# Kernel optimization log

Measured on AMD Instinct MI355X. Metric: run time of the kernel, lower is better.

The kernel has to match this reference:

```python
import jax, jax.numpy as jnp
import numpy as np

N_NODES = 200_000
BATCH = 131_072
D = 128          # memory_dim
E = 64           # edge_feat_dim
T = 64           # time_dim
P = 5            # num_prototypes
LN_EPS = 1e-4


def _xavier(key, shape):
    fan_in, fan_out = shape[-1], shape[-2] if len(shape) > 1 else shape[-1]
    lim = float(np.sqrt(6.0 / (fan_in + fan_out)))
    return jax.random.uniform(key, shape, jnp.float32, -lim, lim)


def _ln(x, g, b):
    mu = x.mean(-1, keepdims=True)
    var = ((x - mu) ** 2).mean(-1, keepdims=True)
    return (x - mu) * jax.lax.rsqrt(var + LN_EPS) * g + b


def setup_inputs() -> dict:
    key = jax.random.key(0)
    ks = jax.random.split(key, 14)
    return {
        "node_ids": jax.random.randint(ks[0], (BATCH,), 0, N_NODES),
        "edge_features": jax.random.normal(ks[1], (BATCH, E), jnp.float32),
        "t": jax.random.uniform(ks[2], (BATCH,), jnp.float32),
        "raw_memory": jax.random.normal(ks[3], (N_NODES, D), jnp.float32) * 0.01,
        "all_prototypes": _xavier(ks[4], (N_NODES, P, D)),
        "proto_ln_g": jnp.ones((D,), jnp.float32),
        "proto_ln_b": jnp.zeros((D,), jnp.float32),
        "time_w": jax.random.normal(ks[5], (T,), jnp.float32),
        "time_b": jnp.zeros((T,), jnp.float32),
        "edge_w": _xavier(ks[6], (D, E)),
        "edge_b": jnp.zeros((D,), jnp.float32),
        "query_w": _xavier(ks[7], (D, D + D + T)),
        "query_b": jnp.zeros((D,), jnp.float32),
        "cell_ln_g": jnp.ones((D,), jnp.float32),
        "cell_ln_b": jnp.zeros((D,), jnp.float32),
        "gate_w": _xavier(ks[8], (1, 2 * D + T)),
        "gate_b": jnp.ones((1,), jnp.float32),
        "temperature": jnp.ones((1,), jnp.float32) * 0.1,
    }


def reference(node_ids, edge_features, t, raw_memory, all_prototypes,
              proto_ln_g, proto_ln_b, time_w, time_b, edge_w, edge_b,
              query_w, query_b, cell_ln_g, cell_ln_b, gate_w, gate_b,
              temperature):
    # gather per-interaction state
    raw = raw_memory[node_ids]                                   # [B, D]
    protos = _ln(all_prototypes[node_ids], proto_ln_g, proto_ln_b)  # [B, P, D]
    # projections / time encoding (TimeEncoder: cos(Linear(t)))
    edge = edge_features @ edge_w.T + edge_b                     # [B, D]
    te = jnp.cos(t[:, None] * time_w[None, :] + time_b)          # [B, T]
    # query
    qi = jnp.concatenate([raw, edge, te], axis=-1)               # [B, 2D+T]
    query = jnp.tanh(_ln(qi @ query_w.T + query_b, cell_ln_g, cell_ln_b))
    # cosine similarity over P prototypes
    qn = query / jnp.clip(jnp.linalg.norm(query, axis=-1, keepdims=True), 1e-6)
    pn = protos / jnp.clip(jnp.linalg.norm(protos, axis=-1, keepdims=True), 1e-6)
    sim = jnp.einsum('bd,bpd->bp', qn, pn)
    sim = jnp.clip(sim, -30.0, 30.0)
    temp = jnp.clip(temperature, 0.05, 2.0)
    sim = sim / (temp + 1e-4)
    attn = jnp.nan_to_num(jax.nn.softmax(sim, axis=-1), nan=0.0, posinf=0.0, neginf=0.0)
    # candidate memory + gate
    cand = jnp.clip(jnp.einsum('bp,bpd->bd', attn, protos), -5.0, 5.0)
    gi = jnp.clip(jnp.concatenate([raw, cand, te], axis=-1), -100.0, 100.0)
    gate = jax.nn.sigmoid(gi @ gate_w.T + gate_b)                # [B, 1]
    upd = (1.0 - gate) * raw + gate * cand
    upd = jnp.clip(_ln(upd, cell_ln_g, cell_ln_b), -10.0, 10.0)
    return upd
```

## Files before the change

kernel.cpp:

```cpp
#include <hip/hip_runtime.h>

#define D 128
#define EDIM 64
#define TDIM 64
#define KTOT 256
#define NP 5
#define LN_EPS 1e-4f
#define WSB_OFF 33024

typedef float v4f __attribute__((ext_vector_type(4)));
typedef float f32x4 __attribute__((ext_vector_type(4)));
typedef short bf16x8 __attribute__((ext_vector_type(8)));

__device__ __forceinline__ float clipf(float x, float lo, float hi) {
    return fminf(fmaxf(x, lo), hi);
}

__device__ __forceinline__ unsigned short bf16rne(float x) {
    unsigned int u = __float_as_uint(x);
    unsigned int r = (u + 0x7fffu + ((u >> 16) & 1u)) >> 16;
    return (unsigned short)r;
}
__device__ __forceinline__ float bf16tof(unsigned short h) {
    return __uint_as_float(((unsigned int)h) << 16);
}

template <int CTRL>
__device__ __forceinline__ float dpp_addstep(float v) {
    int o = __builtin_amdgcn_update_dpp(0, __float_as_int(v), CTRL, 0xF, 0xF, true);
    return v + __int_as_float(o);
}
__device__ __forceinline__ float qred16(float v) {
    v = dpp_addstep<0xB1>(v);
    v = dpp_addstep<0x4E>(v);
    v = dpp_addstep<0x124>(v);
    v = dpp_addstep<0x128>(v);
    return v;
}

__global__ void k0_fold(const float* __restrict__ qw, const float* __restrict__ qb,
                        const float* __restrict__ ew, const float* __restrict__ eb,
                        const float* __restrict__ pg, const float* __restrict__ pb,
                        float* __restrict__ ws) {
    const int d = threadIdx.x;
    const int bk = blockIdx.x;
    float* Wt = ws;
    float* c0 = ws + KTOT * D;
    float* cc = c0 + D;
    if (bk < 128) {
        Wt[bk * D + d] = qw[d * 320 + bk];
    } else if (bk < 192) {
        const int e = bk - 128;
        const float4* qrow = (const float4*)(qw + d * 320 + 128);
        float s = 0.f;
        #pragma unroll
        for (int g = 0; g < 32; ++g) {
            float4 q = qrow[g];
            s = fmaf(q.x, ew[(4 * g + 0) * EDIM + e], s);
            s = fmaf(q.y, ew[(4 * g + 1) * EDIM + e], s);
            s = fmaf(q.z, ew[(4 * g + 2) * EDIM + e], s);
            s = fmaf(q.w, ew[(4 * g + 3) * EDIM + e], s);
        }
        Wt[bk * D + d] = s;
    } else if (bk < 256) {
        Wt[bk * D + d] = qw[d * 320 + 256 + (bk - 192)];
    } else if (bk == 256) {
        const float4* qrow = (const float4*)(qw + d * 320 + 128);
        const float4* eb4 = (const float4*)eb;
        float s = qb[d];
        #pragma unroll
        for (int g = 0; g < 32; ++g) {
            float4 q = qrow[g], e4 = eb4[g];
            s = fmaf(q.x, e4.x, s); s = fmaf(q.y, e4.y, s);
            s = fmaf(q.z, e4.z, s); s = fmaf(q.w, e4.w, s);
        }
        c0[d] = s;
    } else {
        if (d == 0) { float s = 0.f; for (int i = 0; i < D; ++i) s = fmaf(pg[i], pg[i], s); cc[0] = s; }
        if (d == 1) { float s = 0.f; for (int i = 0; i < D; ++i) s = fmaf(pg[i], pb[i], s); cc[1] = s; }
        if (d == 2) { float s = 0.f; for (int i = 0; i < D; ++i) s = fmaf(pb[i], pb[i], s); cc[2] = s; }
    }
}

__global__ void k0b_pack(float* __restrict__ ws) {
    const int kb = blockIdx.x >> 3;
    const int nt = blockIdx.x & 7;
    const int l = threadIdx.x;
    const float* Wt = ws;
    const int col = nt * 16 + (l & 15);
    const int kbase = kb * 32 + (l >> 4) * 8;
    bf16x8 hi, lo;
    #pragma unroll
    for (int j = 0; j < 8; ++j) {
        float x = Wt[(kbase + j) * D + col];
        unsigned short h = bf16rne(x);
        hi[j] = (short)h;
        lo[j] = (short)bf16rne(x - bf16tof(h));
    }
    bf16x8* outp = (bf16x8*)(ws + WSB_OFF);
    outp[((kb * 8 + nt) * 2 + 0) * 64 + l] = hi;
    outp[((kb * 8 + nt) * 2 + 1) * 64 + l] = lo;
}

__global__ __launch_bounds__(256, 3)
void k_fused(const int* __restrict__ nids, const float* __restrict__ ef,
             const float* __restrict__ tarr, const float* __restrict__ raw_mem,
             const float* __restrict__ protos,
             const float* __restrict__ pg, const float* __restrict__ pb,
             const float* __restrict__ tw, const float* __restrict__ tb,
             const float* __restrict__ cg, const float* __restrict__ cb,
             const float* __restrict__ gw, const float* __restrict__ gb,
             const float* __restrict__ temp, const float* __restrict__ ws,
             float* __restrict__ out, int Btot) {
    __shared__ bf16x8 Bs[1024];
    __shared__ float cst[960];

    const int tid = threadIdx.x;
    const int lane = tid & 63;
    const int wave = tid >> 6;
    const int m0 = blockIdx.x * 64 + wave * 16;
    const int col = lane & 15;
    const int kg = lane >> 4;

    if (tid < 128) {
        cst[tid] = gw[tid];
        cst[128 + tid] = gw[128 + tid];
    } else {
        const int u = tid - 128;
        if (u < 64) { cst[256 + u] = tw[u]; cst[320 + u] = tb[u]; }
        else        { cst[384 + u - 64] = gw[256 + u - 64]; }
    }

    const int elemA = min(m0 + col, Btot - 1);
    const int nidA = nids[elemA];
    const float* rawpA = raw_mem + (size_t)nidA * D + kg * 8;
    const float* efpA = ef + (size_t)elemA * EDIM + kg * 8;
    const float tvalA = tarr[elemA];
    const bf16x8* wbg = (const bf16x8*)(ws + WSB_OFF);

    f32x4 acc[8];
    #pragma unroll
    for (int nt = 0; nt < 8; ++nt) acc[nt] = (f32x4){0.f, 0.f, 0.f, 0.f};

    bf16x8 s0 = wbg[tid], s1 = wbg[256 + tid], s2 = wbg[512 + tid], s3 = wbg[768 + tid];
    v4f xa0 = *(const v4f*)rawpA;
    v4f xa1 = *(const v4f*)(rawpA + 4);

    #pragma unroll 1
    for (int kb = 0; kb < 8; ++kb) {
        __syncthreads();
        Bs[tid] = s0; Bs[256 + tid] = s1; Bs[512 + tid] = s2; Bs[768 + tid] = s3;
        __syncthreads();
        v4f xn0 = xa0, xn1 = xa1;
        if (kb < 7) {
            const int kn = kb + 1;
            const bf16x8* wn = wbg + kn * 1024;
            s0 = wn[tid]; s1 = wn[256 + tid]; s2 = wn[512 + tid]; s3 = wn[768 + tid];
            if (kn < 4) {
                xn0 = *(const v4f*)(rawpA + kn * 32);
                xn1 = *(const v4f*)(rawpA + kn * 32 + 4);
            } else if (kn < 6) {
                xn0 = *(const v4f*)(efpA + (kn - 4) * 32);
                xn1 = *(const v4f*)(efpA + (kn - 4) * 32 + 4);
            } else {
                const int u0 = (kn - 6) * 32 + kg * 8;
                v4f wa = *(const v4f*)(tw + u0);
                v4f wb2 = *(const v4f*)(tw + u0 + 4);
                v4f ba = *(const v4f*)(tb + u0);
                v4f bb2 = *(const v4f*)(tb + u0 + 4);
                #pragma unroll
                for (int j = 0; j < 4; ++j) xn0[j] = __cosf(fmaf(tvalA, wa[j], ba[j]));
                #pragma unroll
                for (int j = 0; j < 4; ++j) xn1[j] = __cosf(fmaf(tvalA, wb2[j], bb2[j]));
            }
        }
        bf16x8 ahi, alo;
        #pragma unroll
        for (int j = 0; j < 4; ++j) {
            unsigned short h = bf16rne(xa0[j]);
            ahi[j] = (short)h;
            alo[j] = (short)bf16rne(xa0[j] - bf16tof(h));
        }
        #pragma unroll
        for (int j = 0; j < 4; ++j) {
            unsigned short h = bf16rne(xa1[j]);
            ahi[4 + j] = (short)h;
            alo[4 + j] = (short)bf16rne(xa1[j] - bf16tof(h));
        }
        #pragma unroll
        for (int nt = 0; nt < 8; ++nt) {
            bf16x8 bhi = Bs[(nt * 2 + 0) * 64 + lane];
            bf16x8 blo = Bs[(nt * 2 + 1) * 64 + lane];
            acc[nt] = __builtin_amdgcn_mfma_f32_16x16x32_bf16(ahi, bhi, acc[nt], 0, 0, 0);
            acc[nt] = __builtin_amdgcn_mfma_f32_16x16x32_bf16(ahi, blo, acc[nt], 0, 0, 0);
            acc[nt] = __builtin_amdgcn_mfma_f32_16x16x32_bf16(alo, bhi, acc[nt], 0, 0, 0);
        }
        xa0 = xn0; xa1 = xn1;
    }

    {
        const float* c0 = ws + KTOT * D;
        #pragma unroll
        for (int j = 0; j < 8; ++j) {
            const float cv = c0[j * 16 + col];
            acc[j][0] += cv; acc[j][1] += cv; acc[j][2] += cv; acc[j][3] += cv;
        }
    }
    const float sbb = (ws + KTOT * D + D)[2];
    const float tempc = fminf(fmaxf(temp[0], 0.05f), 2.0f) + 1e-4f;
    const float its = 1.0f / tempc;
    const float gbias = gb[0];

    float pg8[8], pb8[8], cg8[8], cb8[8];
    #pragma unroll
    for (int j = 0; j < 8; ++j) {
        const int dd = j * 16 + col;
        pg8[j] = pg[dd]; pb8[j] = pb[dd];
        cg8[j] = cg[dd]; cb8[j] = cb[dd];
    }

    #pragma unroll
    for (int r = 0; r < 4; ++r) {
        const int erow = m0 + kg * 4 + r;
        const bool act = (erow < Btot);
        const int ebb = act ? erow : Btot - 1;
        const int nid = nids[ebb];
        const float* rawrow = raw_mem + (size_t)nid * D;
        const float* prow = protos + (size_t)nid * (NP * D);
        const float tval = tarr[ebb];

        float qv[8], rawv[8];
        #pragma unroll
        for (int j = 0; j < 8; ++j) {
            qv[j] = acc[j][r];
            rawv[j] = rawrow[j * 16 + col];
        }
        float pxv[NP][8];
        #pragma unroll
        for (int p = 0; p < NP; ++p) {
            #pragma unroll
            for (int j = 0; j < 8; ++j) pxv[p][j] = prow[p * D + j * 16 + col];
        }

        float gsum = 0.f;
        #pragma unroll
        for (int j = 0; j < 8; ++j)
            gsum = fmaf(cst[j * 16 + col], clipf(rawv[j], -100.f, 100.f), gsum);
        #pragma unroll
        for (int j = 0; j < 4; ++j) {
            const int u = col * 4 + j;
            gsum = fmaf(cst[384 + u], __cosf(fmaf(tval, cst[256 + u], cst[320 + u])), gsum);
        }

        float sx = 0.f;
        #pragma unroll
        for (int j = 0; j < 8; ++j) sx += qv[j];
        sx = qred16(sx);
        const float mu = sx * (1.f / D);
        float sv = 0.f;
        #pragma unroll
        for (int j = 0; j < 8; ++j) { float a = qv[j] - mu; sv = fmaf(a, a, sv); }
        sv = qred16(sv);
        const float rsq = __builtin_amdgcn_rsqf(sv * (1.f / D) + LN_EPS);

        float ssq = 0.f;
        #pragma unroll
        for (int j = 0; j < 8; ++j) {
            float x = fmaf((qv[j] - mu) * rsq, cg8[j], cb8[j]);
            float e2x = __expf(2.f * x);
            float th = 1.f - 2.f * __builtin_amdgcn_rcpf(e2x + 1.f);
            qv[j] = th;
            ssq = fmaf(th, th, ssq);
        }
        ssq = qred16(ssq);
        const float invq = __builtin_amdgcn_rcpf(fmaxf(sqrtf(ssq), 1e-6f));

        float aqg = 0.f, aqb = 0.f;
        #pragma unroll
        for (int j = 0; j < 8; ++j) {
            float qn = qv[j] * invq;
            float qg = qn * pg8[j];
            aqg += qg;
            aqb = fmaf(qn, pb8[j], aqb);
            qv[j] = qg;
        }
        aqg = qred16(aqg);
        aqb = qred16(aqb);

        float mups[NP], rsps[NP], simv[NP];
        #pragma unroll
        for (int p = 0; p < NP; ++p) {
            float s_x = 0.f, sxx = 0.f, sqgx = 0.f;
            #pragma unroll
            for (int j = 0; j < 8; ++j) {
                float x = pxv[p][j];
                s_x += x;
                sxx = fmaf(x, x, sxx);
                sqgx = fmaf(qv[j], x, sqgx);
            }
            s_x = qred16(s_x); sxx = qred16(sxx); sqgx = qred16(sqgx);
            const float mup = s_x * (1.f / D);
            const float varp = sxx * (1.f / D) - mup * mup;
            const float rsp = __builtin_amdgcn_rsqf(varp + LN_EPS);
            float sz2 = 0.f, szb = 0.f;
            #pragma unroll
            for (int j = 0; j < 8; ++j) {
                float z = (pxv[p][j] - mup) * pg8[j];
                sz2 = fmaf(z, z, sz2);
                szb = fmaf(z, pb8[j], szb);
            }
            sz2 = qred16(sz2); szb = qred16(szb);
            const float dot = fmaf(rsp, sqgx - mup * aqg, aqb);
            float nrm2 = fmaf(rsp * rsp, sz2, fmaf(2.f * rsp, szb, sbb));
            nrm2 = fmaxf(nrm2, 0.f);
            const float inv = __builtin_amdgcn_rcpf(fmaxf(sqrtf(nrm2), 1e-6f));
            mups[p] = mup;
            rsps[p] = rsp;
            simv[p] = clipf(dot * inv, -30.f, 30.f) * its;
        }

        float mx = fmaxf(fmaxf(fmaxf(simv[0], simv[1]), fmaxf(simv[2], simv[3])), simv[4]);
        float wp[NP];
        float Z = 0.f;
        #pragma unroll
        for (int p = 0; p < NP; ++p) { float ev = __expf(simv[p] - mx); wp[p] = ev; Z += ev; }
        const float iZ = 1.f / Z;
        float a0 = 0.f, a1 = 0.f;
        #pragma unroll
        for (int p = 0; p < NP; ++p) {
            float at = wp[p] * iZ;
            a0 += at;
            float w = at * rsps[p];
            a1 = fmaf(w, mups[p], a1);
            wp[p] = w;
        }

        float S8[8];
        #pragma unroll
        for (int j = 0; j < 8; ++j) S8[j] = 0.f;
        #pragma unroll
        for (int p = 0; p < NP; ++p) {
            #pragma unroll
            for (int j = 0; j < 8; ++j) S8[j] = fmaf(wp[p], pxv[p][j], S8[j]);
        }
        float gc = gsum;
        #pragma unroll
        for (int j = 0; j < 8; ++j) {
            float cnd = clipf(fmaf(pg8[j], S8[j] - a1, pb8[j] * a0), -5.f, 5.f);
            gc = fmaf(cst[128 + j * 16 + col], cnd, gc);
            S8[j] = cnd;
        }
        gc = qred16(gc);
        const float gpre = gc + gbias;
        const float gate = __builtin_amdgcn_rcpf(1.f + __expf(-gpre));

        float su = 0.f, ssu = 0.f;
        #pragma unroll
        for (int j = 0; j < 8; ++j) {
            float u = fmaf(gate, S8[j] - rawv[j], rawv[j]);
            S8[j] = u;
            su += u;
            ssu = fmaf(u, u, ssu);
        }
        su = qred16(su);
        ssu = qred16(ssu);
        const float muu = su * (1.f / D);
        const float varu = ssu * (1.f / D) - muu * muu;
        const float rsu = __builtin_amdgcn_rsqf(varu + LN_EPS);

        if (act) {
            float* orow = out + (size_t)erow * D;
            #pragma unroll
            for (int j = 0; j < 8; ++j) {
                orow[j * 16 + col] = clipf(fmaf((S8[j] - muu) * rsu, cg8[j], cb8[j]), -10.f, 10.f);
            }
        }
    }
}

extern "C" void kernel_launch(void* const* d_in, const int* in_sizes, int n_in,
                              void* d_out, int out_size, void* d_ws, size_t ws_size,
                              hipStream_t stream) {
    const int*   nids = (const int*)d_in[0];
    const float* ef   = (const float*)d_in[1];
    const float* t    = (const float*)d_in[2];
    const float* raw  = (const float*)d_in[3];
    const float* prot = (const float*)d_in[4];
    const float* pg   = (const float*)d_in[5];
    const float* pb   = (const float*)d_in[6];
    const float* tw   = (const float*)d_in[7];
    const float* tb   = (const float*)d_in[8];
    const float* ew   = (const float*)d_in[9];
    const float* eb   = (const float*)d_in[10];
    const float* qw   = (const float*)d_in[11];
    const float* qb   = (const float*)d_in[12];
    const float* cg   = (const float*)d_in[13];
    const float* cb   = (const float*)d_in[14];
    const float* gw   = (const float*)d_in[15];
    const float* gb   = (const float*)d_in[16];
    const float* temp = (const float*)d_in[17];
    float* ws  = (float*)d_ws;
    float* out = (float*)d_out;
    const int Btot = in_sizes[0];

    hipLaunchKernelGGL(k0_fold, dim3(258), dim3(128), 0, stream,
                       qw, qb, ew, eb, pg, pb, ws);
    hipLaunchKernelGGL(k0b_pack, dim3(64), dim3(64), 0, stream, ws);
    hipLaunchKernelGGL(k_fused, dim3((Btot + 63) / 64), dim3(256), 0, stream,
                       nids, ef, t, raw, prot, pg, pb, tw, tb, cg, cb, gw, gb, temp, ws, out, Btot);
}
```

Before: 120.5 us.

## Permute weight columns so each lane owns 8 contiguous features; vectorize epilogue loads

```diff
diff --git a/kernel.cpp b/kernel.cpp
--- a/kernel.cpp
+++ b/kernel.cpp
@@ -87,12 +87,12 @@
     const int nt = blockIdx.x & 7;
     const int l = threadIdx.x;
     const float* Wt = ws;
-    const int col = nt * 16 + (l & 15);
+    const int dlog = (l & 15) * 8 + nt;
     const int kbase = kb * 32 + (l >> 4) * 8;
     bf16x8 hi, lo;
     #pragma unroll
     for (int j = 0; j < 8; ++j) {
-        float x = Wt[(kbase + j) * D + col];
+        float x = Wt[(kbase + j) * D + dlog];
         unsigned short h = bf16rne(x);
         hi[j] = (short)h;
         lo[j] = (short)bf16rne(x - bf16tof(h));
@@ -113,7 +113,6 @@
              const float* __restrict__ temp, const float* __restrict__ ws,
              float* __restrict__ out, int Btot) {
     __shared__ bf16x8 Bs[1024];
-    __shared__ float cst[960];
 
     const int tid = threadIdx.x;
     const int lane = tid & 63;
@@ -121,15 +120,6 @@
     const int m0 = blockIdx.x * 64 + wave * 16;
     const int col = lane & 15;
     const int kg = lane >> 4;
-
-    if (tid < 128) {
-        cst[tid] = gw[tid];
-        cst[128 + tid] = gw[128 + tid];
-    } else {
-        const int u = tid - 128;
-        if (u < 64) { cst[256 + u] = tw[u]; cst[320 + u] = tb[u]; }
-        else        { cst[384 + u - 64] = gw[256 + u - 64]; }
-    }
 
     const int elemA = min(m0 + col, Btot - 1);
     const int nidA = nids[elemA];
@@ -198,11 +188,14 @@
         xa0 = xn0; xa1 = xn1;
     }
 
+    const int d0 = col * 8;
+
     {
-        const float* c0 = ws + KTOT * D;
-        #pragma unroll
-        for (int j = 0; j < 8; ++j) {
-            const float cv = c0[j * 16 + col];
+        const v4f c0a = *(const v4f*)(ws + KTOT * D + d0);
+        const v4f c0b = *(const v4f*)(ws + KTOT * D + d0 + 4);
+        #pragma unroll
+        for (int j = 0; j < 8; ++j) {
+            const float cv = (j < 4) ? c0a[j] : c0b[j - 4];
             acc[j][0] += cv; acc[j][1] += cv; acc[j][2] += cv; acc[j][3] += cv;
         }
     }
@@ -211,13 +204,22 @@
     const float its = 1.0f / tempc;
     const float gbias = gb[0];
 
-    float pg8[8], pb8[8], cg8[8], cb8[8];
-    #pragma unroll
-    for (int j = 0; j < 8; ++j) {
-        const int dd = j * 16 + col;
-        pg8[j] = pg[dd]; pb8[j] = pb[dd];
-        cg8[j] = cg[dd]; cb8[j] = cb[dd];
-    }
+    const v4f pgA = *(const v4f*)(pg + d0), pgB = *(const v4f*)(pg + d0 + 4);
+    const v4f pbA = *(const v4f*)(pb + d0), pbB = *(const v4f*)(pb + d0 + 4);
+    const v4f cgA = *(const v4f*)(cg + d0), cgB = *(const v4f*)(cg + d0 + 4);
+    const v4f cbA = *(const v4f*)(cb + d0), cbB = *(const v4f*)(cb + d0 + 4);
+    const v4f grA = *(const v4f*)(gw + d0), grB = *(const v4f*)(gw + d0 + 4);
+    const v4f gcA = *(const v4f*)(gw + D + d0), gcB = *(const v4f*)(gw + D + d0 + 4);
+    const v4f twc = *(const v4f*)(tw + col * 4);
+    const v4f tbc = *(const v4f*)(tb + col * 4);
+    const v4f gwt = *(const v4f*)(gw + 2 * D + col * 4);
+
+#define PG8(j) ((j) < 4 ? pgA[(j)] : pgB[(j) - 4])
+#define PB8(j) ((j) < 4 ? pbA[(j)] : pbB[(j) - 4])
+#define CG8(j) ((j) < 4 ? cgA[(j)] : cgB[(j) - 4])
+#define CB8(j) ((j) < 4 ? cbA[(j)] : cbB[(j) - 4])
+#define GR8(j) ((j) < 4 ? grA[(j)] : grB[(j) - 4])
+#define GC8(j) ((j) < 4 ? gcA[(j)] : gcB[(j) - 4])
 
     #pragma unroll
     for (int r = 0; r < 4; ++r) {
@@ -229,28 +231,29 @@
         const float* prow = protos + (size_t)nid * (NP * D);
         const float tval = tarr[ebb];
 
+        const v4f ra = *(const v4f*)(rawrow + d0);
+        const v4f rb = *(const v4f*)(rawrow + d0 + 4);
+        v4f pA[NP], pB[NP];
+        #pragma unroll
+        for (int p = 0; p < NP; ++p) {
+            pA[p] = *(const v4f*)(prow + p * D + d0);
+            pB[p] = *(const v4f*)(prow + p * D + d0 + 4);
+        }
+
         float qv[8], rawv[8];
         #pragma unroll
         for (int j = 0; j < 8; ++j) {
             qv[j] = acc[j][r];
-            rawv[j] = rawrow[j * 16 + col];
-        }
-        float pxv[NP][8];
-        #pragma unroll
-        for (int p = 0; p < NP; ++p) {
-            #pragma unroll
-            for (int j = 0; j < 8; ++j) pxv[p][j] = prow[p * D + j * 16 + col];
+            rawv[j] = (j < 4) ? ra[j] : rb[j - 4];
         }
 
         float gsum = 0.f;
         #pragma unroll
         for (int j = 0; j < 8; ++j)
-            gsum = fmaf(cst[j * 16 + col], clipf(rawv[j], -100.f, 100.f), gsum);
-        #pragma unroll
-        for (int j = 0; j < 4; ++j) {
-            const int u = col * 4 + j;
-            gsum = fmaf(cst[384 + u], __cosf(fmaf(tval, cst[256 + u], cst[320 + u])), gsum);
-        }
+            gsum = fmaf(GR8(j), clipf(rawv[j], -100.f, 100.f), gsum);
+        #pragma unroll
+        for (int j = 0; j < 4; ++j)
+            gsum = fmaf(gwt[j], __cosf(fmaf(tval, twc[j], tbc[j])), gsum);
 
         float sx = 0.f;
         #pragma unroll
@@ -266,7 +269,7 @@
         float ssq = 0.f;
         #pragma unroll
         for (int j = 0; j < 8; ++j) {
-            float x = fmaf((qv[j] - mu) * rsq, cg8[j], cb8[j]);
+            float x = fmaf((qv[j] - mu) * rsq, CG8(j), CB8(j));
             float e2x = __expf(2.f * x);
             float th = 1.f - 2.f * __builtin_amdgcn_rcpf(e2x + 1.f);
             qv[j] = th;
@@ -279,9 +282,9 @@
         #pragma unroll
         for (int j = 0; j < 8; ++j) {
             float qn = qv[j] * invq;
-            float qg = qn * pg8[j];
+            float qg = qn * PG8(j);
             aqg += qg;
-            aqb = fmaf(qn, pb8[j], aqb);
+            aqb = fmaf(qn, PB8(j), aqb);
             qv[j] = qg;
         }
         aqg = qred16(aqg);
@@ -293,7 +296,7 @@
             float s_x = 0.f, sxx = 0.f, sqgx = 0.f;
             #pragma unroll
             for (int j = 0; j < 8; ++j) {
-                float x = pxv[p][j];
+                float x = (j < 4) ? pA[p][j] : pB[p][j - 4];
                 s_x += x;
                 sxx = fmaf(x, x, sxx);
                 sqgx = fmaf(qv[j], x, sqgx);
@@ -305,9 +308,10 @@
             float sz2 = 0.f, szb = 0.f;
             #pragma unroll
             for (int j = 0; j < 8; ++j) {
-                float z = (pxv[p][j] - mup) * pg8[j];
+                float x = (j < 4) ? pA[p][j] : pB[p][j - 4];
+                float z = (x - mup) * PG8(j);
                 sz2 = fmaf(z, z, sz2);
-                szb = fmaf(z, pb8[j], szb);
+                szb = fmaf(z, PB8(j), szb);
             }
             sz2 = qred16(sz2); szb = qred16(szb);
             const float dot = fmaf(rsp, sqgx - mup * aqg, aqb);
@@ -341,13 +345,16 @@
         #pragma unroll
         for (int p = 0; p < NP; ++p) {
             #pragma unroll
-            for (int j = 0; j < 8; ++j) S8[j] = fmaf(wp[p], pxv[p][j], S8[j]);
+            for (int j = 0; j < 8; ++j) {
+                float x = (j < 4) ? pA[p][j] : pB[p][j - 4];
+                S8[j] = fmaf(wp[p], x, S8[j]);
+            }
         }
         float gc = gsum;
         #pragma unroll
         for (int j = 0; j < 8; ++j) {
-            float cnd = clipf(fmaf(pg8[j], S8[j] - a1, pb8[j] * a0), -5.f, 5.f);
-            gc = fmaf(cst[128 + j * 16 + col], cnd, gc);
+            float cnd = clipf(fmaf(PG8(j), S8[j] - a1, PB8(j) * a0), -5.f, 5.f);
+            gc = fmaf(GC8(j), cnd, gc);
             S8[j] = cnd;
         }
         gc = qred16(gc);
@@ -369,11 +376,16 @@
         const float rsu = __builtin_amdgcn_rsqf(varu + LN_EPS);
 
         if (act) {
-            float* orow = out + (size_t)erow * D;
+            float* orow = out + (size_t)erow * D + d0;
+            v4f o0, o1;
             #pragma unroll
-            for (int j = 0; j < 8; ++j) {
-                orow[j * 16 + col] = clipf(fmaf((S8[j] - muu) * rsu, cg8[j], cb8[j]), -10.f, 10.f);
-            }
+            for (int j = 0; j < 4; ++j)
+                o0[j] = clipf(fmaf((S8[j] - muu) * rsu, CG8(j), CB8(j)), -10.f, 10.f);
+            #pragma unroll
+            for (int j = 4; j < 8; ++j)
+                o1[j - 4] = clipf(fmaf((S8[j] - muu) * rsu, CG8(j), CB8(j)), -10.f, 10.f);
+            *(v4f*)orow = o0;
+            *(v4f*)(orow + 4) = o1;
         }
     }
 }
```

Result: slower. 126.7 us (+5.2%).

## Double-buffer weight tiles in LDS and prefetch first row's gathers before GEMM

Applied to the files above, without the earlier changes.

```diff
diff --git a/kernel.cpp b/kernel.cpp
--- a/kernel.cpp
+++ b/kernel.cpp
@@ -87,12 +87,12 @@
     const int nt = blockIdx.x & 7;
     const int l = threadIdx.x;
     const float* Wt = ws;
-    const int col = nt * 16 + (l & 15);
+    const int colp = nt * 16 + (l & 15);
     const int kbase = kb * 32 + (l >> 4) * 8;
     bf16x8 hi, lo;
     #pragma unroll
     for (int j = 0; j < 8; ++j) {
-        float x = Wt[(kbase + j) * D + col];
+        float x = Wt[(kbase + j) * D + colp];
         unsigned short h = bf16rne(x);
         hi[j] = (short)h;
         lo[j] = (short)bf16rne(x - bf16tof(h));
@@ -112,8 +112,8 @@
              const float* __restrict__ gw, const float* __restrict__ gb,
              const float* __restrict__ temp, const float* __restrict__ ws,
              float* __restrict__ out, int Btot) {
-    __shared__ bf16x8 Bs[1024];
-    __shared__ float cst[960];
+    __shared__ bf16x8 Bs[2048];
+    __shared__ float cst[448];
 
     const int tid = threadIdx.x;
     const int lane = tid & 63;
@@ -146,11 +146,34 @@
     v4f xa0 = *(const v4f*)rawpA;
     v4f xa1 = *(const v4f*)(rawpA + 4);
 
+    const int erow0 = m0 + kg * 4;
+    int nid_r[4];
+    float tval_r[4];
+    #pragma unroll
+    for (int r = 0; r < 4; ++r) {
+        const int eb = min(erow0 + r, Btot - 1);
+        nid_r[r] = nids[eb];
+        tval_r[r] = tarr[eb];
+    }
+    float pre_raw[8], pre_px[NP][8];
+    {
+        const float* rawrow0 = raw_mem + (size_t)nid_r[0] * D;
+        const float* prow0 = protos + (size_t)nid_r[0] * (NP * D);
+        #pragma unroll
+        for (int j = 0; j < 8; ++j) pre_raw[j] = rawrow0[j * 16 + col];
+        #pragma unroll
+        for (int p = 0; p < NP; ++p) {
+            #pragma unroll
+            for (int j = 0; j < 8; ++j) pre_px[p][j] = prow0[p * D + j * 16 + col];
+        }
+    }
+
+    Bs[tid] = s0; Bs[256 + tid] = s1; Bs[512 + tid] = s2; Bs[768 + tid] = s3;
+    __syncthreads();
+
     #pragma unroll 1
     for (int kb = 0; kb < 8; ++kb) {
-        __syncthreads();
-        Bs[tid] = s0; Bs[256 + tid] = s1; Bs[512 + tid] = s2; Bs[768 + tid] = s3;
-        __syncthreads();
+        const int cur = (kb & 1) << 10;
         v4f xn0 = xa0, xn1 = xa1;
         if (kb < 7) {
             const int kn = kb + 1;
@@ -189,11 +212,17 @@
         }
         #pragma unroll
         for (int nt = 0; nt < 8; ++nt) {
-            bf16x8 bhi = Bs[(nt * 2 + 0) * 64 + lane];
-            bf16x8 blo = Bs[(nt * 2 + 1) * 64 + lane];
+            bf16x8 bhi = Bs[cur + (nt * 2 + 0) * 64 + lane];
+            bf16x8 blo = Bs[cur + (nt * 2 + 1) * 64 + lane];
             acc[nt] = __builtin_amdgcn_mfma_f32_16x16x32_bf16(ahi, bhi, acc[nt], 0, 0, 0);
             acc[nt] = __builtin_amdgcn_mfma_f32_16x16x32_bf16(ahi, blo, acc[nt], 0, 0, 0);
             acc[nt] = __builtin_amdgcn_mfma_f32_16x16x32_bf16(alo, bhi, acc[nt], 0, 0, 0);
+        }
+        if (kb < 7) {
+            const int nxt = cur ^ 1024;
+            Bs[nxt + tid] = s0; Bs[nxt + 256 + tid] = s1;
+            Bs[nxt + 512 + tid] = s2; Bs[nxt + 768 + tid] = s3;
+            __syncthreads();
         }
         xa0 = xn0; xa1 = xn1;
     }
@@ -223,34 +252,31 @@
     for (int r = 0; r < 4; ++r) {
         const int erow = m0 + kg * 4 + r;
         const bool act = (erow < Btot);
-        const int ebb = act ? erow : Btot - 1;
-        const int nid = nids[ebb];
+        const int nid = nid_r[r];
+        const float tval = tval_r[r];
         const float* rawrow = raw_mem + (size_t)nid * D;
         const float* prow = protos + (size_t)nid * (NP * D);
-        const float tval = tarr[ebb];
-
-        float qv[8], rawv[8];
-        #pragma unroll
-        for (int j = 0; j < 8; ++j) {
-            qv[j] = acc[j][r];
-            rawv[j] = rawrow[j * 16 + col];
-        }
-        float pxv[NP][8];
-        #pragma unroll
-        for (int p = 0; p < NP; ++p) {
-            #pragma unroll
-            for (int j = 0; j < 8; ++j) pxv[p][j] = prow[p * D + j * 16 + col];
-        }
-
-        float gsum = 0.f;
-        #pragma unroll
-        for (int j = 0; j < 8; ++j)
-            gsum = fmaf(cst[j * 16 + col], clipf(rawv[j], -100.f, 100.f), gsum);
-        #pragma unroll
-        for (int j = 0; j < 4; ++j) {
-            const int u = col * 4 + j;
-            gsum = fmaf(cst[384 + u], __cosf(fmaf(tval, cst[256 + u], cst[320 + u])), gsum);
-        }
+
+        float rawv[8], pxv[NP][8];
+        if (r == 0) {
+            #pragma unroll
+            for (int j = 0; j < 8; ++j) rawv[j] = pre_raw[j];
+            #pragma unroll
+            for (int p = 0; p < NP; ++p)
+                #pragma unroll
+                for (int j = 0; j < 8; ++j) pxv[p][j] = pre_px[p][j];
+        } else {
+            #pragma unroll
+            for (int j = 0; j < 8; ++j) rawv[j] = rawrow[j * 16 + col];
+            #pragma unroll
+            for (int p = 0; p < NP; ++p)
+                #pragma unroll
+                for (int j = 0; j < 8; ++j) pxv[p][j] = prow[p * D + j * 16 + col];
+        }
+
+        float qv[8];
+        #pragma unroll
+        for (int j = 0; j < 8; ++j) qv[j] = acc[j][r];
 
         float sx = 0.f;
         #pragma unroll
@@ -286,6 +312,19 @@
         }
         aqg = qred16(aqg);
         aqb = qred16(aqb);
+
+        float gsum = 0.f;
+        {
+            #pragma unroll
+            for (int j = 0; j < 8; ++j)
+                gsum = fmaf(cst[j * 16 + col], clipf(rawv[j], -100.f, 100.f), gsum);
+            const v4f twc = *(const v4f*)&cst[256 + col * 4];
+            const v4f tbc = *(const v4f*)&cst[320 + col * 4];
+            const v4f gwt = *(const v4f*)&cst[384 + col * 4];
+            #pragma unroll
+            for (int j = 0; j < 4; ++j)
+                gsum = fmaf(gwt[j], __cosf(fmaf(tval, twc[j], tbc[j])), gsum);
+        }
 
         float mups[NP], rsps[NP], simv[NP];
         #pragma unroll
```

Result: slower. 125.4 us (+4.1%).

## Double-buffer weight tiles in LDS via direct global-to-LDS loads

Applied to the files above, without the earlier changes.

```diff
diff --git a/kernel.cpp b/kernel.cpp
--- a/kernel.cpp
+++ b/kernel.cpp
@@ -87,12 +87,12 @@
     const int nt = blockIdx.x & 7;
     const int l = threadIdx.x;
     const float* Wt = ws;
-    const int col = nt * 16 + (l & 15);
+    const int colp = nt * 16 + (l & 15);
     const int kbase = kb * 32 + (l >> 4) * 8;
     bf16x8 hi, lo;
     #pragma unroll
     for (int j = 0; j < 8; ++j) {
-        float x = Wt[(kbase + j) * D + col];
+        float x = Wt[(kbase + j) * D + colp];
         unsigned short h = bf16rne(x);
         hi[j] = (short)h;
         lo[j] = (short)bf16rne(x - bf16tof(h));
@@ -112,8 +112,8 @@
              const float* __restrict__ gw, const float* __restrict__ gb,
              const float* __restrict__ temp, const float* __restrict__ ws,
              float* __restrict__ out, int Btot) {
-    __shared__ bf16x8 Bs[1024];
-    __shared__ float cst[960];
+    __shared__ bf16x8 Bs[2048];
+    __shared__ float cst[448];
 
     const int tid = threadIdx.x;
     const int lane = tid & 63;
@@ -142,20 +142,34 @@
     #pragma unroll
     for (int nt = 0; nt < 8; ++nt) acc[nt] = (f32x4){0.f, 0.f, 0.f, 0.f};
 
-    bf16x8 s0 = wbg[tid], s1 = wbg[256 + tid], s2 = wbg[512 + tid], s3 = wbg[768 + tid];
+#define STAGE_B(KB, BUF) { \
+        const bf16x8* wn_ = wbg + (KB) * 1024; \
+        __builtin_amdgcn_global_load_lds( \
+            (const __attribute__((address_space(1))) unsigned int*)(wn_ + 0 * 256 + tid), \
+            (__attribute__((address_space(3))) unsigned int*)&Bs[(BUF) + 0 * 256 + wave * 64], 16, 0, 0); \
+        __builtin_amdgcn_global_load_lds( \
+            (const __attribute__((address_space(1))) unsigned int*)(wn_ + 1 * 256 + tid), \
+            (__attribute__((address_space(3))) unsigned int*)&Bs[(BUF) + 1 * 256 + wave * 64], 16, 0, 0); \
+        __builtin_amdgcn_global_load_lds( \
+            (const __attribute__((address_space(1))) unsigned int*)(wn_ + 2 * 256 + tid), \
+            (__attribute__((address_space(3))) unsigned int*)&Bs[(BUF) + 2 * 256 + wave * 64], 16, 0, 0); \
+        __builtin_amdgcn_global_load_lds( \
+            (const __attribute__((address_space(1))) unsigned int*)(wn_ + 3 * 256 + tid), \
+            (__attribute__((address_space(3))) unsigned int*)&Bs[(BUF) + 3 * 256 + wave * 64], 16, 0, 0); \
+    }
+
+    STAGE_B(0, 0)
     v4f xa0 = *(const v4f*)rawpA;
     v4f xa1 = *(const v4f*)(rawpA + 4);
+    __syncthreads();
 
     #pragma unroll 1
     for (int kb = 0; kb < 8; ++kb) {
-        __syncthreads();
-        Bs[tid] = s0; Bs[256 + tid] = s1; Bs[512 + tid] = s2; Bs[768 + tid] = s3;
-        __syncthreads();
+        const int cur = (kb & 1) << 10;
         v4f xn0 = xa0, xn1 = xa1;
         if (kb < 7) {
             const int kn = kb + 1;
-            const bf16x8* wn = wbg + kn * 1024;
-            s0 = wn[tid]; s1 = wn[256 + tid]; s2 = wn[512 + tid]; s3 = wn[768 + tid];
+            STAGE_B(kn, cur ^ 1024)
             if (kn < 4) {
                 xn0 = *(const v4f*)(rawpA + kn * 32);
                 xn1 = *(const v4f*)(rawpA + kn * 32 + 4);
@@ -189,12 +203,13 @@
         }
         #pragma unroll
         for (int nt = 0; nt < 8; ++nt) {
-            bf16x8 bhi = Bs[(nt * 2 + 0) * 64 + lane];
-            bf16x8 blo = Bs[(nt * 2 + 1) * 64 + lane];
+            bf16x8 bhi = Bs[cur + (nt * 2 + 0) * 64 + lane];
+            bf16x8 blo = Bs[cur + (nt * 2 + 1) * 64 + lane];
             acc[nt] = __builtin_amdgcn_mfma_f32_16x16x32_bf16(ahi, bhi, acc[nt], 0, 0, 0);
             acc[nt] = __builtin_amdgcn_mfma_f32_16x16x32_bf16(ahi, blo, acc[nt], 0, 0, 0);
             acc[nt] = __builtin_amdgcn_mfma_f32_16x16x32_bf16(alo, bhi, acc[nt], 0, 0, 0);
         }
+        if (kb < 7) __syncthreads();
         xa0 = xn0; xa1 = xn1;
     }
 
@@ -229,28 +244,17 @@
         const float* prow = protos + (size_t)nid * (NP * D);
         const float tval = tarr[ebb];
 
-        float qv[8], rawv[8];
-        #pragma unroll
-        for (int j = 0; j < 8; ++j) {
-            qv[j] = acc[j][r];
-            rawv[j] = rawrow[j * 16 + col];
-        }
-        float pxv[NP][8];
-        #pragma unroll
-        for (int p = 0; p < NP; ++p) {
+        float rawv[8], pxv[NP][8];
+        #pragma unroll
+        for (int j = 0; j < 8; ++j) rawv[j] = rawrow[j * 16 + col];
+        #pragma unroll
+        for (int p = 0; p < NP; ++p)
             #pragma unroll
             for (int j = 0; j < 8; ++j) pxv[p][j] = prow[p * D + j * 16 + col];
-        }
-
-        float gsum = 0.f;
-        #pragma unroll
-        for (int j = 0; j < 8; ++j)
-            gsum = fmaf(cst[j * 16 + col], clipf(rawv[j], -100.f, 100.f), gsum);
-        #pragma unroll
-        for (int j = 0; j < 4; ++j) {
-            const int u = col * 4 + j;
-            gsum = fmaf(cst[384 + u], __cosf(fmaf(tval, cst[256 + u], cst[320 + u])), gsum);
-        }
+
+        float qv[8];
+        #pragma unroll
+        for (int j = 0; j < 8; ++j) qv[j] = acc[j][r];
 
         float sx = 0.f;
         #pragma unroll
@@ -286,6 +290,19 @@
         }
         aqg = qred16(aqg);
         aqb = qred16(aqb);
+
+        float gsum = 0.f;
+        {
+            #pragma unroll
+            for (int j = 0; j < 8; ++j)
+                gsum = fmaf(cst[j * 16 + col], clipf(rawv[j], -100.f, 100.f), gsum);
+            const v4f twc = *(const v4f*)&cst[256 + col * 4];
+            const v4f tbc = *(const v4f*)&cst[320 + col * 4];
+            const v4f gwt = *(const v4f*)&cst[384 + col * 4];
+            #pragma unroll
+            for (int j = 0; j < 4; ++j)
+                gsum = fmaf(gwt[j], __cosf(fmaf(tval, twc[j], tbc[j])), gsum);
+        }
 
         float mups[NP], rsps[NP], simv[NP];
         #pragma unroll
```

Result: slower. 125.8 us (+4.4%).
